# Performance work log

Hardware: AMD Instinct MI355X
Metric: run time of the kernel (lower is better)

Reference implementation:

```python
import jax, jax.numpy as jnp
import numpy as np

N_NODES = 100000
N_EDGES = 1250000
D = 64


def _sage_conv(x, src, dst, W_l, b_l, W_r, n_nodes):
    # message = x[src]; scatter-mean onto dst; then lin_l(mean) + lin_r(x)
    msg = x[src]                                               # [E, D]
    agg = jax.ops.segment_sum(msg, dst, num_segments=n_nodes)  # [N, D]
    cnt = jax.ops.segment_sum(jnp.ones((src.shape[0],), x.dtype), dst,
                              num_segments=n_nodes)            # [N]
    mean = agg / jnp.maximum(cnt, 1.0)[:, None]
    return mean @ W_l + b_l + x @ W_r


def setup_inputs() -> dict:
    key = jax.random.key(0)
    ks = jax.random.split(key, 8)
    s = 1.0 / np.sqrt(D)
    x = jax.random.normal(ks[0], (N_NODES, D), dtype=jnp.float32)
    edge_index = jax.random.randint(ks[1], (2, N_EDGES), 0, N_NODES, dtype=jnp.int32)
    W_l1 = jax.random.normal(ks[2], (D, D), dtype=jnp.float32) * s
    b_l1 = jnp.zeros((D,), jnp.float32)
    W_r1 = jax.random.normal(ks[3], (D, D), dtype=jnp.float32) * s
    W_l2 = jax.random.normal(ks[4], (D, D), dtype=jnp.float32) * s
    b_l2 = jnp.zeros((D,), jnp.float32)
    W_r2 = jax.random.normal(ks[5], (D, D), dtype=jnp.float32) * s
    return {"x": x, "edge_index": edge_index,
            "W_l1": W_l1, "b_l1": b_l1, "W_r1": W_r1,
            "W_l2": W_l2, "b_l2": b_l2, "W_r2": W_r2}


def reference(x, edge_index, W_l1, b_l1, W_r1, W_l2, b_l2, W_r2):
    src, dst = edge_index[0], edge_index[1]
    n = x.shape[0]
    h = jax.nn.relu(_sage_conv(x, src, dst, W_l1, b_l1, W_r1, n))
    return _sage_conv(h, src, dst, W_l2, b_l2, W_r2, n)
```

## Files before the change

kernel.cpp:

```cpp
#include <hip/hip_runtime.h>

#define N_NODES 100000
#define N_EDGES 1250000
#define D 64
#define ZERO_NODE N_NODES

#define BIN_SHIFT 9
#define BIN_NODES 512
#define NBINS ((N_NODES + BIN_NODES - 1) >> BIN_SHIFT)
#define BIN_CAP 7168
#define BIN_SLAB 8704
#define CHUNK 2048

#define SLAB_INTS (NBINS * BIN_SLAB)

typedef __attribute__((ext_vector_type(8))) short short8;
typedef __attribute__((ext_vector_type(4))) float f32x4;

__device__ inline unsigned short f2bf(float f) {
    unsigned int u = __float_as_uint(f);
    unsigned int r = (u + 0x7fffu + ((u >> 16) & 1u)) >> 16;
    return (unsigned short)r;
}
__device__ inline float bfl(unsigned int u) { return __uint_as_float(u << 16); }
__device__ inline float bfh(unsigned int u) { return __uint_as_float(u & 0xffff0000u); }

__global__ __launch_bounds__(256)
void convert_zero_kernel(const float4* __restrict__ xin, ushort4* __restrict__ xb,
                         int n4, int* __restrict__ bin_cnt,
                         unsigned int* __restrict__ xb_zrow,
                         unsigned int* __restrict__ h_zrow,
                         const float* __restrict__ Wl1, const float* __restrict__ Wr1,
                         const float* __restrict__ Wl2, const float* __restrict__ Wr2,
                         unsigned short* __restrict__ wt) {
    int i = blockIdx.x * 256 + threadIdx.x;
    if (i < n4) {
        float4 v = xin[i];
        ushort4 u;
        u.x = f2bf(v.x); u.y = f2bf(v.y); u.z = f2bf(v.z); u.w = f2bf(v.w);
        xb[i] = u;
    }
    if (i < NBINS) bin_cnt[i] = 0;
    if (i < 32) { xb_zrow[i] = 0u; h_zrow[i] = 0u; }
    if (i < 2 * 64 * 128) {
        int layer = i >> 13;
        int n = (i >> 7) & 63;
        int k = i & 127;
        const float* W = layer ? (k < 64 ? Wl2 : Wr2) : (k < 64 ? Wl1 : Wr1);
        float v = W[(k & 63) * D + n];
        wt[i] = f2bf(v);
    }
}

__global__ __launch_bounds__(1024)
void bin_partition_kernel(const int* __restrict__ src, const int* __restrict__ dst,
                          int* __restrict__ bin_cnt, int* __restrict__ binslab) {
    __shared__ int lhist[NBINS];
    __shared__ int lstart[NBINS];
    __shared__ int lbase[NBINS];
    __shared__ int lcur[NBINS];
    __shared__ int wsum[4];
    __shared__ int sval[CHUNK];
    __shared__ int sdst[CHUNK];

    const int t = threadIdx.x;
    const int lane = t & 63, wave = t >> 6;
    const int e0 = blockIdx.x * CHUNK;
    int cnt = N_EDGES - e0; if (cnt > CHUNK) cnt = CHUNK;

    if (t < NBINS) lhist[t] = 0;
    __syncthreads();

    for (int i = t; i < cnt; i += 1024)
        atomicAdd(&lhist[dst[e0 + i] >> BIN_SHIFT], 1);
    __syncthreads();

    int h = (t < NBINS) ? lhist[t] : 0;
    int v = h;
    for (int off = 1; off < 64; off <<= 1) {
        int u = __shfl_up(v, off);
        if (lane >= off) v += u;
    }
    if (lane == 63 && wave < 4) wsum[wave] = v;
    __syncthreads();
    if (t < NBINS) {
        int wpre = 0;
        for (int w = 0; w < wave; ++w) wpre += wsum[w];
        int excl = v + wpre - h;
        lstart[t] = excl;
        lcur[t] = excl;
        lbase[t] = (h > 0) ? atomicAdd(&bin_cnt[t], h) : 0;
    }
    __syncthreads();

    for (int i = t; i < cnt; i += 1024) {
        int d = dst[e0 + i];
        int s = src[e0 + i];
        int b = d >> BIN_SHIFT;
        int slot = atomicAdd(&lcur[b], 1);
        int rank = slot - lstart[b];
        sval[slot] = (s << BIN_SHIFT) | (d & (BIN_NODES - 1));
        int gp = lbase[b] + rank;
        sdst[slot] = (gp < BIN_CAP) ? (b * BIN_CAP + gp) : -1;
    }
    __syncthreads();

    for (int i = t; i < cnt; i += 1024) {
        int dd = sdst[i];
        if (dd >= 0) binslab[dd] = sval[i];
    }
}

__global__ __launch_bounds__(1024)
void bin_build_kernel(const int* __restrict__ binslab, const int* __restrict__ bin_cnt,
                      int* __restrict__ deg_out, int* __restrict__ rstart_out,
                      int* __restrict__ slabs) {
    __shared__ int hist[BIN_NODES];
    __shared__ int cur[BIN_NODES];
    __shared__ int wsum[8];

    const int b = blockIdx.x;
    const int t = threadIdx.x;
    const int lane = t & 63, wave = t >> 6;
    int cnt = bin_cnt[b]; if (cnt > BIN_CAP) cnt = BIN_CAP;
    const int s0 = b * BIN_CAP;
    const int nb0 = b << BIN_SHIFT;

    if (t < BIN_NODES) hist[t] = 0;
    __syncthreads();

    for (int i = t; i < cnt; i += 1024)
        atomicAdd(&hist[binslab[s0 + i] & (BIN_NODES - 1)], 1);
    __syncthreads();

    int h = (t < BIN_NODES) ? hist[t] : 0;
    int p = (h + 3) & ~3;
    int v = p;
    for (int off = 1; off < 64; off <<= 1) {
        int u = __shfl_up(v, off);
        if (lane >= off) v += u;
    }
    if (lane == 63 && wave < 8) wsum[wave] = v;
    __syncthreads();
    if (t < BIN_NODES) {
        int wpre = 0;
        for (int w = 0; w < wave; ++w) wpre += wsum[w];
        int excl = v + wpre - p;
        int rs = b * BIN_SLAB + excl;
        cur[t] = rs;
        int n = nb0 + t;
        if (n < N_NODES) {
            deg_out[n] = h;
            rstart_out[n] = rs;
            for (int j = h; j < p; ++j) slabs[rs + j] = ZERO_NODE;
        }
    }
    __syncthreads();

    for (int i = t; i < cnt; i += 1024) {
        int pk = binslab[s0 + i];
        int pos = atomicAdd(&cur[pk & (BIN_NODES - 1)], 1);
        slabs[pos] = pk >> BIN_SHIFT;
    }
}

template <typename TOUT>
__global__ __launch_bounds__(256, 8)
void fused_layer_kernel(const unsigned short* __restrict__ xin,
                        const int* __restrict__ rstart,
                        const int* __restrict__ deg,
                        const int* __restrict__ sorted_src,
                        const unsigned short* __restrict__ wt,
                        const float* __restrict__ bl,
                        TOUT* __restrict__ out,
                        int relu) {
    __shared__ __align__(16) unsigned short sA[32][136];

    const uint4* __restrict__ xin128 = (const uint4*)xin;

    const int tid = threadIdx.x;
    const int row0 = blockIdx.x * 32;

    const int wave = tid >> 6;
    const int lane = tid & 63;
    const int s8 = lane >> 3;
    const int f4 = lane & 7;

    for (int r = wave; r < 32; r += 4) {
        int n = row0 + r;
        int dg = deg[n];
        int pdg = (dg + 3) & ~3;
        int st = rstart[n];
        uint4 xraw = xin128[(size_t)n * 8 + f4];

        float a0 = 0.f, a1 = 0.f, a2 = 0.f, a3 = 0.f;
        float a4 = 0.f, a5 = 0.f, a6 = 0.f, a7 = 0.f;

        for (int base = 0; base < pdg; base += 64) {
            int m = pdg - base; if (m > 64) m = 64;
            int idx = ZERO_NODE;
            if (lane < m) idx = sorted_src[st + base + lane];
            int quads = m >> 2;
            int eCur = __shfl(idx, s8);
            uint4 uCur = xin128[(size_t)eCur * 8 + f4];
            int t = 0;
            for (; t + 2 < quads; t += 2) {
                int eN = __shfl(idx, 4 * (t + 2) + s8);
                uint4 uN = xin128[(size_t)eN * 8 + f4];
                a0 += bfl(uCur.x); a1 += bfh(uCur.x);
                a2 += bfl(uCur.y); a3 += bfh(uCur.y);
                a4 += bfl(uCur.z); a5 += bfh(uCur.z);
                a6 += bfl(uCur.w); a7 += bfh(uCur.w);
                uCur = uN;
            }
            a0 += bfl(uCur.x); a1 += bfh(uCur.x);
            a2 += bfl(uCur.y); a3 += bfh(uCur.y);
            a4 += bfl(uCur.z); a5 += bfh(uCur.z);
            a6 += bfl(uCur.w); a7 += bfh(uCur.w);
        }

        a0 += __shfl_xor(a0, 8);  a1 += __shfl_xor(a1, 8);
        a2 += __shfl_xor(a2, 8);  a3 += __shfl_xor(a3, 8);
        a4 += __shfl_xor(a4, 8);  a5 += __shfl_xor(a5, 8);
        a6 += __shfl_xor(a6, 8);  a7 += __shfl_xor(a7, 8);
        a0 += __shfl_xor(a0, 16); a1 += __shfl_xor(a1, 16);
        a2 += __shfl_xor(a2, 16); a3 += __shfl_xor(a3, 16);
        a4 += __shfl_xor(a4, 16); a5 += __shfl_xor(a5, 16);
        a6 += __shfl_xor(a6, 16); a7 += __shfl_xor(a7, 16);
        a0 += __shfl_xor(a0, 32); a1 += __shfl_xor(a1, 32);
        a2 += __shfl_xor(a2, 32); a3 += __shfl_xor(a3, 32);
        a4 += __shfl_xor(a4, 32); a5 += __shfl_xor(a5, 32);
        a6 += __shfl_xor(a6, 32); a7 += __shfl_xor(a7, 32);

        float inv = 1.0f / (float)(dg > 0 ? dg : 1);
        if (lane < 8) {
            uint4 pk;
            pk.x = (unsigned int)f2bf(a0 * inv) | ((unsigned int)f2bf(a1 * inv) << 16);
            pk.y = (unsigned int)f2bf(a2 * inv) | ((unsigned int)f2bf(a3 * inv) << 16);
            pk.z = (unsigned int)f2bf(a4 * inv) | ((unsigned int)f2bf(a5 * inv) << 16);
            pk.w = (unsigned int)f2bf(a6 * inv) | ((unsigned int)f2bf(a7 * inv) << 16);
            *(uint4*)&sA[r][f4 * 8] = pk;
            *(uint4*)&sA[r][64 + f4 * 8] = xraw;
        }
    }
    __syncthreads();

    const int tm = wave & 1;
    const int tn0 = (wave >> 1) * 2;
    const int mrow = tm * 16 + (lane & 15);
    const int kq = (lane >> 4) * 8;

    short8 afr[4];
#pragma unroll
    for (int kk = 0; kk < 4; ++kk)
        afr[kk] = *(const short8*)&sA[mrow][kk * 32 + kq];

#pragma unroll
    for (int ti = 0; ti < 2; ++ti) {
        const int tn = tn0 + ti;
        const int col = tn * 16 + (lane & 15);
        float bias = bl[col];
        f32x4 acc = {bias, bias, bias, bias};
#pragma unroll
        for (int kk = 0; kk < 4; ++kk) {
            short8 bfr = *(const short8*)&wt[col * 128 + kk * 32 + kq];
            acc = __builtin_amdgcn_mfma_f32_16x16x32_bf16(afr[kk], bfr, acc, 0, 0, 0);
        }
        const int r0 = row0 + tm * 16 + (lane >> 4) * 4;
#pragma unroll
        for (int reg = 0; reg < 4; ++reg) {
            float o = relu ? fmaxf(acc[reg], 0.f) : acc[reg];
            if constexpr (__hip_internal::is_same<TOUT, unsigned short>::value)
                out[(size_t)(r0 + reg) * D + col] = f2bf(o);
            else
                out[(size_t)(r0 + reg) * D + col] = o;
        }
    }
}

extern "C" void kernel_launch(void* const* d_in, const int* in_sizes, int n_in,
                              void* d_out, int out_size, void* d_ws, size_t ws_size,
                              hipStream_t stream) {
    const float* x   = (const float*)d_in[0];
    const int*   ei  = (const int*)d_in[1];
    const float* Wl1 = (const float*)d_in[2];
    const float* b1  = (const float*)d_in[3];
    const float* Wr1 = (const float*)d_in[4];
    const float* Wl2 = (const float*)d_in[5];
    const float* b2  = (const float*)d_in[6];
    const float* Wr2 = (const float*)d_in[7];

    const int* src = ei;
    const int* dst = ei + N_EDGES;

    int* slabs   = (int*)d_ws;
    int* deg     = slabs + SLAB_INTS;
    int* rstart  = deg + N_NODES;
    int* bin_cnt = rstart + N_NODES;
    unsigned short* wt_all = (unsigned short*)(bin_cnt + 256);
    unsigned short* wt1 = wt_all;
    unsigned short* wt2 = wt_all + 64 * 128;
    unsigned short* h = wt_all + 2 * 64 * 128;
    float* out = (float*)d_out;
    unsigned short* xb = (unsigned short*)d_out;
    int* binslab = (int*)d_out + 4 * 1024 * 1024;

    const int dense_blocks = N_NODES / 32;
    const int conv4 = N_NODES * D / 4;
    const int part_blocks = (N_EDGES + CHUNK - 1) / CHUNK;

    convert_zero_kernel<<<(conv4 + 255) / 256, 256, 0, stream>>>(
        (const float4*)x, (ushort4*)xb, conv4, bin_cnt,
        (unsigned int*)(xb + (size_t)ZERO_NODE * D),
        (unsigned int*)(h + (size_t)ZERO_NODE * D),
        Wl1, Wr1, Wl2, Wr2, wt_all);

    bin_partition_kernel<<<part_blocks, 1024, 0, stream>>>(src, dst, bin_cnt, binslab);
    bin_build_kernel<<<NBINS, 1024, 0, stream>>>(binslab, bin_cnt, deg, rstart, slabs);

    fused_layer_kernel<unsigned short><<<dense_blocks, 256, 0, stream>>>(
        xb, rstart, deg, slabs, wt1, b1, h, 1);
    fused_layer_kernel<float><<<dense_blocks, 256, 0, stream>>>(
        h, rstart, deg, slabs, wt2, b2, out, 0);
}
```

Measured before the change: 226.5 us.

## Restructure neighbor gather: two rows per wave, 8-byte lanes, more loads in flight

The gather-mean phase of the fused SAGE layer is reorganised. Each wave now processes two destination rows at once, and each neighbor row is read by 16 lanes with 8-byte loads, so four neighbors are covered per wave step instead of eight lanes with 16-byte loads. The loop is unrolled to issue four independent gathers per iteration with split accumulators, and fewer shuffle-reduction stages are needed. The aim is more memory-level parallelism to hide random gather latency. The cost is narrower per-lane loads, more registers, and imbalance when the two rows have different degrees.

```diff
diff --git a/kernel.cpp b/kernel.cpp
--- a/kernel.cpp
+++ b/kernel.cpp
@@ -22,8 +22,12 @@
     unsigned int r = (u + 0x7fffu + ((u >> 16) & 1u)) >> 16;
     return (unsigned short)r;
 }
-__device__ inline float bfl(unsigned int u) { return __uint_as_float(u << 16); }
-__device__ inline float bfh(unsigned int u) { return __uint_as_float(u & 0xffff0000u); }
+__device__ inline void acc_bf4(float4& c, uint2 u) {
+    c.x += __uint_as_float(u.x << 16);
+    c.y += __uint_as_float(u.x & 0xffff0000u);
+    c.z += __uint_as_float(u.y << 16);
+    c.w += __uint_as_float(u.y & 0xffff0000u);
+}
 
 __global__ __launch_bounds__(256)
 void convert_zero_kernel(const float4* __restrict__ xin, ushort4* __restrict__ xb,
@@ -176,71 +180,116 @@
                         int relu) {
     __shared__ __align__(16) unsigned short sA[32][136];
 
-    const uint4* __restrict__ xin128 = (const uint4*)xin;
+    const uint2* __restrict__ xin64 = (const uint2*)xin;
 
     const int tid = threadIdx.x;
     const int row0 = blockIdx.x * 32;
 
     const int wave = tid >> 6;
     const int lane = tid & 63;
-    const int s8 = lane >> 3;
-    const int f4 = lane & 7;
-
-    for (int r = wave; r < 32; r += 4) {
-        int n = row0 + r;
-        int dg = deg[n];
-        int pdg = (dg + 3) & ~3;
-        int st = rstart[n];
-        uint4 xraw = xin128[(size_t)n * 8 + f4];
-
-        float a0 = 0.f, a1 = 0.f, a2 = 0.f, a3 = 0.f;
-        float a4 = 0.f, a5 = 0.f, a6 = 0.f, a7 = 0.f;
-
-        for (int base = 0; base < pdg; base += 64) {
-            int m = pdg - base; if (m > 64) m = 64;
-            int idx = ZERO_NODE;
-            if (lane < m) idx = sorted_src[st + base + lane];
-            int quads = m >> 2;
-            int eCur = __shfl(idx, s8);
-            uint4 uCur = xin128[(size_t)eCur * 8 + f4];
-            int t = 0;
-            for (; t + 2 < quads; t += 2) {
-                int eN = __shfl(idx, 4 * (t + 2) + s8);
-                uint4 uN = xin128[(size_t)eN * 8 + f4];
-                a0 += bfl(uCur.x); a1 += bfh(uCur.x);
-                a2 += bfl(uCur.y); a3 += bfh(uCur.y);
-                a4 += bfl(uCur.z); a5 += bfh(uCur.z);
-                a6 += bfl(uCur.w); a7 += bfh(uCur.w);
-                uCur = uN;
+    const int q  = lane >> 4;
+    const int f2 = lane & 15;
+
+#pragma unroll
+    for (int j = 0; j < 4; ++j) {
+        const int rA = wave * 8 + 2 * j;
+        const int rB = rA + 1;
+        const int nA = row0 + rA, nB = row0 + rB;
+
+        int dgA = deg[nA], dgB = deg[nB];
+        int stA = rstart[nA], stB = rstart[nB];
+        int pdgA = (dgA + 3) & ~3, pdgB = (dgB + 3) & ~3;
+        int mA = pdgA > 64 ? 64 : pdgA;
+        int mB = pdgB > 64 ? 64 : pdgB;
+
+        int idxA = ZERO_NODE, idxB = ZERO_NODE;
+        if (lane < mA) idxA = sorted_src[stA + lane];
+        if (lane < mB) idxB = sorted_src[stB + lane];
+        uint2 xrawA = xin64[(size_t)nA * 16 + f2];
+        uint2 xrawB = xin64[(size_t)nB * 16 + f2];
+
+        float4 cA0 = make_float4(0.f, 0.f, 0.f, 0.f);
+        float4 cA1 = make_float4(0.f, 0.f, 0.f, 0.f);
+        float4 cB0 = make_float4(0.f, 0.f, 0.f, 0.f);
+        float4 cB1 = make_float4(0.f, 0.f, 0.f, 0.f);
+
+        const int quadsA = mA >> 2, quadsB = mB >> 2;
+        const int quads = quadsA > quadsB ? quadsA : quadsB;
+        int t = 0;
+        for (; t + 2 <= quads; t += 2) {
+            int eA0 = __shfl(idxA, 4 * t + q);
+            int eA1 = __shfl(idxA, 4 * t + 4 + q);
+            int eB0 = __shfl(idxB, 4 * t + q);
+            int eB1 = __shfl(idxB, 4 * t + 4 + q);
+            uint2 uA0 = xin64[(size_t)eA0 * 16 + f2];
+            uint2 uA1 = xin64[(size_t)eA1 * 16 + f2];
+            uint2 uB0 = xin64[(size_t)eB0 * 16 + f2];
+            uint2 uB1 = xin64[(size_t)eB1 * 16 + f2];
+            acc_bf4(cA0, uA0); acc_bf4(cA1, uA1);
+            acc_bf4(cB0, uB0); acc_bf4(cB1, uB1);
+        }
+        for (; t < quads; ++t) {
+            int eA0 = __shfl(idxA, 4 * t + q);
+            int eB0 = __shfl(idxB, 4 * t + q);
+            uint2 uA0 = xin64[(size_t)eA0 * 16 + f2];
+            uint2 uB0 = xin64[(size_t)eB0 * 16 + f2];
+            acc_bf4(cA0, uA0); acc_bf4(cB0, uB0);
+        }
+
+        if (__builtin_expect(pdgA > 64, 0)) {
+            for (int base = 64; base < pdgA; base += 64) {
+                int m = pdgA - base; if (m > 64) m = 64;
+                int idx = ZERO_NODE;
+                if (lane < m) idx = sorted_src[stA + base + lane];
+                int qds = m >> 2;
+                for (int tt = 0; tt < qds; ++tt) {
+                    int e = __shfl(idx, 4 * tt + q);
+                    acc_bf4(cA0, xin64[(size_t)e * 16 + f2]);
+                }
             }
-            a0 += bfl(uCur.x); a1 += bfh(uCur.x);
-            a2 += bfl(uCur.y); a3 += bfh(uCur.y);
-            a4 += bfl(uCur.z); a5 += bfh(uCur.z);
-            a6 += bfl(uCur.w); a7 += bfh(uCur.w);
-        }
-
-        a0 += __shfl_xor(a0, 8);  a1 += __shfl_xor(a1, 8);
-        a2 += __shfl_xor(a2, 8);  a3 += __shfl_xor(a3, 8);
-        a4 += __shfl_xor(a4, 8);  a5 += __shfl_xor(a5, 8);
-        a6 += __shfl_xor(a6, 8);  a7 += __shfl_xor(a7, 8);
-        a0 += __shfl_xor(a0, 16); a1 += __shfl_xor(a1, 16);
-        a2 += __shfl_xor(a2, 16); a3 += __shfl_xor(a3, 16);
-        a4 += __shfl_xor(a4, 16); a5 += __shfl_xor(a5, 16);
-        a6 += __shfl_xor(a6, 16); a7 += __shfl_xor(a7, 16);
-        a0 += __shfl_xor(a0, 32); a1 += __shfl_xor(a1, 32);
-        a2 += __shfl_xor(a2, 32); a3 += __shfl_xor(a3, 32);
-        a4 += __shfl_xor(a4, 32); a5 += __shfl_xor(a5, 32);
-        a6 += __shfl_xor(a6, 32); a7 += __shfl_xor(a7, 32);
-
-        float inv = 1.0f / (float)(dg > 0 ? dg : 1);
-        if (lane < 8) {
-            uint4 pk;
-            pk.x = (unsigned int)f2bf(a0 * inv) | ((unsigned int)f2bf(a1 * inv) << 16);
-            pk.y = (unsigned int)f2bf(a2 * inv) | ((unsigned int)f2bf(a3 * inv) << 16);
-            pk.z = (unsigned int)f2bf(a4 * inv) | ((unsigned int)f2bf(a5 * inv) << 16);
-            pk.w = (unsigned int)f2bf(a6 * inv) | ((unsigned int)f2bf(a7 * inv) << 16);
-            *(uint4*)&sA[r][f4 * 8] = pk;
-            *(uint4*)&sA[r][64 + f4 * 8] = xraw;
+        }
+        if (__builtin_expect(pdgB > 64, 0)) {
+            for (int base = 64; base < pdgB; base += 64) {
+                int m = pdgB - base; if (m > 64) m = 64;
+                int idx = ZERO_NODE;
+                if (lane < m) idx = sorted_src[stB + base + lane];
+                int qds = m >> 2;
+                for (int tt = 0; tt < qds; ++tt) {
+                    int e = __shfl(idx, 4 * tt + q);
+                    acc_bf4(cB0, xin64[(size_t)e * 16 + f2]);
+                }
+            }
+        }
+
+        float aAx = cA0.x + cA1.x, aAy = cA0.y + cA1.y;
+        float aAz = cA0.z + cA1.z, aAw = cA0.w + cA1.w;
+        float aBx = cB0.x + cB1.x, aBy = cB0.y + cB1.y;
+        float aBz = cB0.z + cB1.z, aBw = cB0.w + cB1.w;
+
+        aAx += __shfl_xor(aAx, 16); aAy += __shfl_xor(aAy, 16);
+        aAz += __shfl_xor(aAz, 16); aAw += __shfl_xor(aAw, 16);
+        aBx += __shfl_xor(aBx, 16); aBy += __shfl_xor(aBy, 16);
+        aBz += __shfl_xor(aBz, 16); aBw += __shfl_xor(aBw, 16);
+        aAx += __shfl_xor(aAx, 32); aAy += __shfl_xor(aAy, 32);
+        aAz += __shfl_xor(aAz, 32); aAw += __shfl_xor(aAw, 32);
+        aBx += __shfl_xor(aBx, 32); aBy += __shfl_xor(aBy, 32);
+        aBz += __shfl_xor(aBz, 32); aBw += __shfl_xor(aBw, 32);
+
+        float invA = 1.0f / (float)(dgA > 0 ? dgA : 1);
+        float invB = 1.0f / (float)(dgB > 0 ? dgB : 1);
+        if (q == 0) {
+            unsigned int p0 = (unsigned int)f2bf(aAx * invA) |
+                              ((unsigned int)f2bf(aAy * invA) << 16);
+            unsigned int p1 = (unsigned int)f2bf(aAz * invA) |
+                              ((unsigned int)f2bf(aAw * invA) << 16);
+            *(uint2*)&sA[rA][f2 * 4] = make_uint2(p0, p1);
+            *(uint2*)&sA[rA][64 + f2 * 4] = xrawA;
+            unsigned int p2 = (unsigned int)f2bf(aBx * invB) |
+                              ((unsigned int)f2bf(aBy * invB) << 16);
+            unsigned int p3 = (unsigned int)f2bf(aBz * invB) |
+                              ((unsigned int)f2bf(aBw * invB) << 16);
+            *(uint2*)&sA[rB][f2 * 4] = make_uint2(p2, p3);
+            *(uint2*)&sA[rB][64 + f2 * 4] = xrawB;
         }
     }
     __syncthreads();
```

Result: faster. 204.1 us (-9.9%).
